# Kernel optimization log

Measured on AMD Instinct MI355X. Metric: run time of the kernel, lower is better.

## Reference

```python
import jax, jax.numpy as jnp
import numpy as np

B, N, C, R = 16, 1024, 256, 8
E = 262144
NUM_SUPER = 32
EPS = 1e-5


def _ln(x, g, b):
    mu = jnp.mean(x, axis=-1, keepdims=True)
    var = jnp.var(x, axis=-1, keepdims=True)
    return (x - mu) / jnp.sqrt(var + EPS) * g + b


def setup_inputs() -> dict:
    key = jax.random.key(0)
    ks = jax.random.split(key, 20)

    def w(k, shape, fan_in):
        return (jax.random.normal(k, shape, jnp.float32) / np.sqrt(fan_in)).astype(jnp.float32)

    return dict(
        x=jax.random.normal(ks[0], (B, N, C), jnp.float32),
        batch_edge_index=jax.random.randint(ks[1], (2, E), 0, B * N),
        batch_edge_types=jax.random.randint(ks[2], (E,), 0, R),
        # cross-modal attention
        Wq=w(ks[3], (C, C), C), bq=jnp.zeros((C,), jnp.float32),
        Wk=w(ks[4], (C, C), C), bk=jnp.zeros((C,), jnp.float32),
        Wv=w(ks[5], (C, C), C), bv=jnp.zeros((C,), jnp.float32),
        Wg=w(ks[6], (2 * C, C), 2 * C), bg=jnp.zeros((C,), jnp.float32),
        ln_attn_g=jnp.ones((C,), jnp.float32), ln_attn_b=jnp.zeros((C,), jnp.float32),
        # confidence net
        Wc1=w(ks[7], (C, C // 2), C), bc1=jnp.zeros((C // 2,), jnp.float32),
        Wc2=w(ks[8], (C // 2, 1), C // 2), bc2=jnp.zeros((1,), jnp.float32),
        # feature mixer
        Wm=w(ks[9], (2 * C, C), 2 * C), bm=jnp.zeros((C,), jnp.float32),
        ln1_g=jnp.ones((C,), jnp.float32), ln1_b=jnp.zeros((C,), jnp.float32),
        # RGCN
        W_rel=w(ks[10], (R, C, C), C),
        W_root=w(ks[11], (C, C), C),
        b_rgcn=jnp.zeros((C,), jnp.float32),
        ln2_g=jnp.ones((C,), jnp.float32), ln2_b=jnp.zeros((C,), jnp.float32),
        # super class head
        Wh=w(ks[12], (C, NUM_SUPER), C), bh=jnp.zeros((NUM_SUPER,), jnp.float32),
    )


def reference(x, batch_edge_index, batch_edge_types,
              Wq, bq, Wk, bk, Wv, bv, Wg, bg, ln_attn_g, ln_attn_b,
              Wc1, bc1, Wc2, bc2, Wm, bm, ln1_g, ln1_b,
              W_rel, W_root, b_rgcn, ln2_g, ln2_b, Wh, bh):
    residual = x
    q = x @ Wq + bq
    k = x @ Wk + bk
    v = x @ Wv + bv
    attn = jax.nn.softmax(jnp.einsum('bnc,bmc->bnm', q, k) / jnp.sqrt(jnp.float32(C)), axis=-1)
    out = jnp.einsum('bnm,bmc->bnc', attn, v)
    gate = jax.nn.sigmoid(jnp.concatenate([out, residual], axis=-1) @ Wg + bg)
    validated = _ln(gate * out + (1.0 - gate) * residual, ln_attn_g, ln_attn_b)

    conf = jax.nn.sigmoid(jax.nn.relu(validated @ Wc1 + bc1) @ Wc2 + bc2)  # [B,N,1]
    weighted = validated * conf
    xm = jax.nn.relu(jnp.concatenate([x, weighted], axis=-1) @ Wm + bm)
    xn = _ln(xm, ln1_g, ln1_b).reshape(B * N, C)

    # RGCNConv (PyG defaults: mean aggregation per relation, root weight, bias)
    src, dst = batch_edge_index[0], batch_edge_index[1]
    h = jnp.einsum('nc,rcd->rnd', xn, W_rel)          # [R, B*N, C] relation-transformed nodes
    msg = h[batch_edge_types, src]                    # [E, C] per-edge gather
    seg = dst * R + batch_edge_types                  # (node, relation) segment id
    cnt = jax.ops.segment_sum(jnp.ones((E,), xn.dtype), seg, num_segments=B * N * R)
    msg = msg / jnp.maximum(cnt[seg], 1.0)[:, None]
    agg = jax.ops.segment_sum(msg, dst, num_segments=B * N)
    x_rgcn = agg + xn @ W_root + b_rgcn
    x_rgcn = jax.nn.relu(_ln(x_rgcn.reshape(B, N, C), ln2_g, ln2_b))

    denom = jnp.maximum(conf.sum(axis=1), 1e-8)       # [B,1]
    pooled = (x_rgcn * conf).sum(axis=1) / denom      # [B,C]
    return pooled @ Wh + bh                           # [B, NUM_SUPER]
```

## Files before the change

kernel.cpp:

```cpp
#include <hip/hip_runtime.h>
#include <hip/hip_bf16.h>

#define B_ 16
#define N_ 1024
#define C_ 256
#define R_ 8
#define E_ 262144
#define NS_ 32
#define BN_ (B_*N_)
#define BNC_ (BN_*C_)

typedef __hip_bfloat16 bf16;
typedef __attribute__((ext_vector_type(4))) float f32x4;
typedef __attribute__((ext_vector_type(8))) short bf16x8;

__device__ __forceinline__ float b2f(bf16 x) { return __bfloat162float(x); }
__device__ __forceinline__ bf16  f2b(float x) { return __float2bfloat16(x); }
__device__ __forceinline__ float us2f(unsigned short u) { return __uint_as_float((unsigned)u << 16); }

__device__ __forceinline__ void gload16(const void* g, void* l) {
    auto gp = (const __attribute__((address_space(1))) void*)(unsigned long long)g;
    auto lp = (__attribute__((address_space(3))) void*)(unsigned)(unsigned long long)l;
    __builtin_amdgcn_global_load_lds(gp, lp, 16, 0, 0);
}

template<int ACT>
__global__ __launch_bounds__(256) void gemm_bf16(
    const bf16* __restrict__ A, int lda, long long sA,
    const bf16* __restrict__ Bm, int ldb, long long sB,
    bf16* __restrict__ Cc, int ldc, long long sC,
    const float* __restrict__ bias, const float* __restrict__ bias2,
    const float* __restrict__ bias3, int K)
{
    __shared__ short sbuf[8704];
    short* As = sbuf;
    short* Bs = sbuf + 4096;
    const int tid = threadIdx.x;
    const int lane = tid & 63, w = tid >> 6;
    const int wr = w >> 1, wc = w & 1;
    const int bm = blockIdx.y * 128, bn = blockIdx.x * 128;
    const bf16* Ab = A + (size_t)blockIdx.z * sA;
    const bf16* Bb = Bm + (size_t)blockIdx.z * sB;
    bf16* Cb = Cc + (size_t)blockIdx.z * sC;

    const int rg = lane >> 2;
    const int kswz = ((lane & 3) ^ ((rg >> 1) & 3)) * 8;

    f32x4 acc[4][4];
    const f32x4 zz = {0.f, 0.f, 0.f, 0.f};
    #pragma unroll
    for (int i = 0; i < 4; ++i)
        #pragma unroll
        for (int j = 0; j < 4; ++j) acc[i][j] = zz;

    const int fr = lane & 15;
    const int fm = lane >> 4;
    const int fslot = (fm ^ ((fr >> 1) & 3)) * 8;

    for (int k0 = 0; k0 < K; k0 += 32) {
        __syncthreads();
        #pragma unroll
        for (int t = 0; t < 2; ++t) {
            gload16(Ab + (size_t)(bm + t*64 + w*16 + rg) * lda + k0 + kswz, As + t*2048 + w*512);
            gload16(Bb + (size_t)(bn + t*64 + w*16 + rg) * ldb + k0 + kswz, Bs + t*2048 + w*512);
        }
        __syncthreads();
        bf16x8 af[4], bfr[4];
        #pragma unroll
        for (int i = 0; i < 4; ++i)
            af[i] = *(const bf16x8*)&As[(wr*64 + i*16 + fr)*32 + fslot];
        #pragma unroll
        for (int j = 0; j < 4; ++j)
            bfr[j] = *(const bf16x8*)&Bs[(wc*64 + j*16 + fr)*32 + fslot];
        #pragma unroll
        for (int i = 0; i < 4; ++i)
            #pragma unroll
            for (int j = 0; j < 4; ++j)
                acc[i][j] = __builtin_amdgcn_mfma_f32_16x16x32_bf16(af[i], bfr[j], acc[i][j], 0, 0, 0);
    }

    const int er = (lane >> 4) * 4, ec = lane & 15;
    #pragma unroll
    for (int half = 0; half < 2; ++half) {
        __syncthreads();
        if (wr == half) {
            #pragma unroll
            for (int j = 0; j < 4; ++j) {
                const int col = bn + wc*64 + j*16 + ec;
                float bvv = 0.0f;
                if (bias) {
                    const int seg = col >> 8;
                    const float* bp = (seg == 0) ? bias : (seg == 1 ? bias2 : bias3);
                    bvv = bp[col & 255];
                }
                #pragma unroll
                for (int i = 0; i < 4; ++i) {
                    #pragma unroll
                    for (int p = 0; p < 4; ++p) {
                        float val = acc[i][j][p] + bvv;
                        if (ACT == 1) val = fmaxf(val, 0.0f);
                        if (ACT == 2) val = 1.0f / (1.0f + __expf(-val));
                        *(bf16*)&sbuf[(i*16 + er + p)*136 + wc*64 + j*16 + ec] = f2b(val);
                    }
                }
            }
        }
        __syncthreads();
        #pragma unroll
        for (int it = 0; it < 4; ++it) {
            const int ch = tid + it*256;
            const int row = ch >> 4, cp = (ch & 15) * 8;
            *(bf16x8*)&Cb[(size_t)(bm + half*64 + row) * ldc + bn + cp] =
                *(const bf16x8*)&sbuf[row*136 + cp];
        }
    }
}

__global__ __launch_bounds__(256) void prep_w_k(
    const float* __restrict__ Wq, const float* __restrict__ Wk, const float* __restrict__ Wv,
    const float* __restrict__ Wg, const float* __restrict__ Wm, const float* __restrict__ Wc1,
    const float* __restrict__ Wrel, const float* __restrict__ Wroot, bf16* __restrict__ WT)
{
    int t = blockIdx.x;
    const float* in; bf16* out; int K, Nn;
    if (t < 192)      { int wsel = t >> 6; t &= 63;
                        in = wsel == 0 ? Wq : (wsel == 1 ? Wk : Wv);
                        out = WT + wsel*65536; K = 256; Nn = 256; }
    else if (t < 320) { t -= 192; in = Wg;  out = WT + 196608; K = 512; Nn = 256; }
    else if (t < 448) { t -= 320; in = Wm;  out = WT + 327680; K = 512; Nn = 256; }
    else if (t < 480) { t -= 448; in = Wc1; out = WT + 458752; K = 256; Nn = 128; }
    else if (t < 992) { t -= 480; int r = t >> 6; t &= 63;
                        in = Wrel + (size_t)r*65536; out = WT + 491520 + r*65536; K = 256; Nn = 256; }
    else              { t -= 992; in = Wroot; out = WT + 491520 + 524288; K = 256; Nn = 256; }
    const int tpr = Nn >> 5;
    const int n0 = (t % tpr) * 32, k0 = (t / tpr) * 32;
    __shared__ float tile[32][33];
    const int tx = threadIdx.x & 31, ty = threadIdx.x >> 5;
    #pragma unroll
    for (int i = 0; i < 4; ++i) {
        int r = ty + i*8;
        tile[r][tx] = in[(size_t)(k0 + r) * Nn + n0 + tx];
    }
    __syncthreads();
    #pragma unroll
    for (int i = 0; i < 4; ++i) {
        int r = ty + i*8;
        out[(size_t)(n0 + r) * K + k0 + tx] = f2b(tile[tx][r]);
    }
}

__global__ __launch_bounds__(256) void vtrans_k(
    const bf16* __restrict__ in, bf16* __restrict__ out)
{
    __shared__ float tile[32][33];
    in  += (size_t)blockIdx.z * 786432 + 512;
    out += (size_t)blockIdx.z * 262144;
    const int n0 = blockIdx.x * 32, k0 = blockIdx.y * 32;
    const int tx = threadIdx.x & 31, ty = threadIdx.x >> 5;
    #pragma unroll
    for (int i = 0; i < 4; ++i) {
        int r = ty + i*8;
        tile[r][tx] = b2f(in[(size_t)(k0 + r) * 768 + n0 + tx]);
    }
    __syncthreads();
    #pragma unroll
    for (int i = 0; i < 4; ++i) {
        int r = ty + i*8;
        out[(size_t)(n0 + r) * 1024 + k0 + tx] = f2b(tile[tx][r]);
    }
}

__global__ __launch_bounds__(256) void cvt_x_k(const float* __restrict__ x,
    bf16* __restrict__ xb, bf16* __restrict__ cat1, bf16* __restrict__ cat2)
{
    const int i4 = (blockIdx.x * 256 + threadIdx.x) * 4;
    const float4 xv = *(const float4*)(x + i4);
    bf16 bv[4] = { f2b(xv.x), f2b(xv.y), f2b(xv.z), f2b(xv.w) };
    const ushort4 pack = *(const ushort4*)bv;
    const int row = i4 >> 8, col = i4 & 255;
    *(ushort4*)(xb + i4) = pack;
    *(ushort4*)(cat1 + (size_t)row * 512 + 256 + col) = pack;
    *(ushort4*)(cat2 + (size_t)row * 512 + col) = pack;
}

__global__ __launch_bounds__(256) void softmax_k(bf16* __restrict__ s)
{
    const int row = blockIdx.x, tid = threadIdx.x;
    const int lane = tid & 63, wid = tid >> 6;
    bf16* rp = s + (size_t)row * 1024 + tid * 4;
    __shared__ float red[8];
    const ushort4 sv = *(const ushort4*)rp;
    float v0 = us2f(sv.x) * 0.0625f, v1 = us2f(sv.y) * 0.0625f;
    float v2 = us2f(sv.z) * 0.0625f, v3 = us2f(sv.w) * 0.0625f;
    float m = fmaxf(fmaxf(v0, v1), fmaxf(v2, v3));
    #pragma unroll
    for (int o = 32; o >= 1; o >>= 1) m = fmaxf(m, __shfl_xor(m, o));
    if (lane == 0) red[wid] = m;
    __syncthreads();
    const float mx = fmaxf(fmaxf(red[0], red[1]), fmaxf(red[2], red[3]));
    float e0 = __expf(v0 - mx), e1 = __expf(v1 - mx), e2 = __expf(v2 - mx), e3 = __expf(v3 - mx);
    float sm = e0 + e1 + e2 + e3;
    #pragma unroll
    for (int o = 32; o >= 1; o >>= 1) sm += __shfl_xor(sm, o);
    if (lane == 0) red[4 + wid] = sm;
    __syncthreads();
    const float inv = 1.0f / (red[4] + red[5] + red[6] + red[7]);
    bf16 ov[4] = { f2b(e0 * inv), f2b(e1 * inv), f2b(e2 * inv), f2b(e3 * inv) };
    *(ushort4*)rp = *(const ushort4*)ov;
}

template<int RELU>
__global__ __launch_bounds__(256) void ln_k(
    const bf16* __restrict__ in, bf16* __restrict__ out,
    const float* __restrict__ g, const float* __restrict__ bta)
{
    const int node = blockIdx.x * 4 + (threadIdx.x >> 6);
    const int lane = threadIdx.x & 63;
    const ushort4 iv = *(const ushort4*)(in + (size_t)node * 256 + lane * 4);
    float v0 = us2f(iv.x), v1 = us2f(iv.y), v2 = us2f(iv.z), v3 = us2f(iv.w);
    float s  = v0 + v1 + v2 + v3;
    float sq = v0*v0 + v1*v1 + v2*v2 + v3*v3;
    #pragma unroll
    for (int o = 32; o >= 1; o >>= 1) { s += __shfl_xor(s, o); sq += __shfl_xor(sq, o); }
    const float mean = s * (1.0f / 256.0f);
    const float var  = sq * (1.0f / 256.0f) - mean * mean;
    const float rs = rsqrtf(var + 1e-5f);
    const float4 gv = *(const float4*)(g + lane * 4);
    const float4 bv = *(const float4*)(bta + lane * 4);
    float y0 = (v0 - mean) * rs * gv.x + bv.x;
    float y1 = (v1 - mean) * rs * gv.y + bv.y;
    float y2 = (v2 - mean) * rs * gv.z + bv.z;
    float y3 = (v3 - mean) * rs * gv.w + bv.w;
    if (RELU) { y0 = fmaxf(y0, 0.f); y1 = fmaxf(y1, 0.f); y2 = fmaxf(y2, 0.f); y3 = fmaxf(y3, 0.f); }
    bf16 ov[4] = { f2b(y0), f2b(y1), f2b(y2), f2b(y3) };
    *(ushort4*)(out + (size_t)node * 256 + lane * 4) = *(const ushort4*)ov;
}

__global__ __launch_bounds__(256) void blend_ln_k(
    const bf16* __restrict__ gate, const bf16* __restrict__ cat1,
    const float* __restrict__ x, bf16* __restrict__ valid,
    const float* __restrict__ g, const float* __restrict__ bta)
{
    const int node = blockIdx.x * 4 + (threadIdx.x >> 6);
    const int lane = threadIdx.x & 63;
    const ushort4 gt4 = *(const ushort4*)(gate + (size_t)node * 256 + lane * 4);
    const ushort4 ao4 = *(const ushort4*)(cat1 + (size_t)node * 512 + lane * 4);
    const float4  xv4 = *(const float4*)(x + (size_t)node * 256 + lane * 4);
    float g0 = us2f(gt4.x), g1 = us2f(gt4.y), g2 = us2f(gt4.z), g3 = us2f(gt4.w);
    float v0 = g0 * us2f(ao4.x) + (1.f - g0) * xv4.x;
    float v1 = g1 * us2f(ao4.y) + (1.f - g1) * xv4.y;
    float v2 = g2 * us2f(ao4.z) + (1.f - g2) * xv4.z;
    float v3 = g3 * us2f(ao4.w) + (1.f - g3) * xv4.w;
    float s  = v0 + v1 + v2 + v3;
    float sq = v0*v0 + v1*v1 + v2*v2 + v3*v3;
    #pragma unroll
    for (int o = 32; o >= 1; o >>= 1) { s += __shfl_xor(s, o); sq += __shfl_xor(sq, o); }
    const float mean = s * (1.0f / 256.0f);
    const float var  = sq * (1.0f / 256.0f) - mean * mean;
    const float rs = rsqrtf(var + 1e-5f);
    const float4 gv = *(const float4*)(g + lane * 4);
    const float4 bv = *(const float4*)(bta + lane * 4);
    bf16 ov[4] = { f2b((v0 - mean) * rs * gv.x + bv.x), f2b((v1 - mean) * rs * gv.y + bv.y),
                   f2b((v2 - mean) * rs * gv.z + bv.z), f2b((v3 - mean) * rs * gv.w + bv.w) };
    *(ushort4*)(valid + (size_t)node * 256 + lane * 4) = *(const ushort4*)ov;
}

__global__ __launch_bounds__(256) void conf_w_k(
    const bf16* __restrict__ t1, const float* __restrict__ Wc2, const float* __restrict__ bc2,
    const bf16* __restrict__ valid, float* __restrict__ conf, bf16* __restrict__ cat2)
{
    const int node = blockIdx.x * 4 + (threadIdx.x >> 6);
    const int lane = threadIdx.x & 63;
    float a = b2f(t1[(size_t)node * 128 + lane]) * Wc2[lane]
            + b2f(t1[(size_t)node * 128 + 64 + lane]) * Wc2[64 + lane];
    #pragma unroll
    for (int o = 32; o >= 1; o >>= 1) a += __shfl_xor(a, o);
    const float c = 1.0f / (1.0f + __expf(-(a + bc2[0])));
    if (lane == 0) conf[node] = c;
    const ushort4 vv = *(const ushort4*)(valid + (size_t)node * 256 + lane * 4);
    bf16 ov[4] = { f2b(us2f(vv.x) * c), f2b(us2f(vv.y) * c), f2b(us2f(vv.z) * c), f2b(us2f(vv.w) * c) };
    *(ushort4*)(cat2 + (size_t)node * 512 + 256 + lane * 4) = *(const ushort4*)ov;
}

__global__ __launch_bounds__(256) void count2_k(
    const int* __restrict__ dst, const int* __restrict__ et,
    int* __restrict__ deg, int* __restrict__ cnt8)
{
    const int e = blockIdx.x * 256 + threadIdx.x;
    if (e < E_) {
        const int d = dst[e];
        atomicAdd(&deg[d], 1);
        atomicAdd(&cnt8[d * 8 + et[e]], 1);
    }
}

__global__ __launch_bounds__(256) void scan_k(
    const int* __restrict__ deg, int* __restrict__ rowptr, int* __restrict__ cursor)
{
    __shared__ int part[256];
    const int tid = threadIdx.x;
    const int base = tid * 64;
    int s = 0;
    for (int i = 0; i < 64; ++i) s += deg[base + i];
    part[tid] = s; __syncthreads();
    for (int off = 1; off < 256; off <<= 1) {
        int t = (tid >= off) ? part[tid - off] : 0;
        __syncthreads();
        part[tid] += t;
        __syncthreads();
    }
    int run = (tid == 0) ? 0 : part[tid - 1];
    for (int i = 0; i < 64; ++i) {
        rowptr[base + i] = run;
        cursor[base + i] = run;
        run += deg[base + i];
    }
    if (tid == 255) rowptr[BN_] = run;
}

__global__ __launch_bounds__(256) void fill_k(
    const int* __restrict__ src, const int* __restrict__ dst, const int* __restrict__ et,
    int* __restrict__ cursor, int* __restrict__ elist)
{
    const int e = blockIdx.x * 256 + threadIdx.x;
    if (e < E_) {
        const int pos = atomicAdd(&cursor[dst[e]], 1);
        elist[pos] = src[e] | (et[e] << 16);
    }
}

__global__ __launch_bounds__(256) void gather_ln_k(
    const int* __restrict__ rowptr, const int* __restrict__ elist,
    const bf16* __restrict__ h, const int* __restrict__ cnt8,
    const float* __restrict__ brg,
    const float* __restrict__ g, const float* __restrict__ bta,
    bf16* __restrict__ xr)
{
    const int node = blockIdx.x * 4 + (threadIdx.x >> 6);
    const int lane = threadIdx.x & 63;
    const int e0 = rowptr[node], e1 = rowptr[node + 1];
    float invc[8];
    #pragma unroll
    for (int r = 0; r < 8; ++r)
        invc[r] = 1.0f / fmaxf((float)cnt8[node * 8 + r], 1.0f);
    float a0 = 0.f, a1 = 0.f, a2 = 0.f, a3 = 0.f;
    for (int e = e0; e < e1; ++e) {
        const int pe = elist[e];
        const int srcn = pe & 0xffff, rel = pe >> 16;
        const float wgt = invc[rel];
        const ushort4 hv = *(const ushort4*)(h + (size_t)srcn * 2304 + rel * 256 + lane * 4);
        a0 += wgt * us2f(hv.x); a1 += wgt * us2f(hv.y);
        a2 += wgt * us2f(hv.z); a3 += wgt * us2f(hv.w);
    }
    const ushort4 rv = *(const ushort4*)(h + (size_t)node * 2304 + 2048 + lane * 4);
    const float4 bg4 = *(const float4*)(brg + lane * 4);
    const float v0 = a0 + us2f(rv.x) + bg4.x, v1 = a1 + us2f(rv.y) + bg4.y;
    const float v2 = a2 + us2f(rv.z) + bg4.z, v3 = a3 + us2f(rv.w) + bg4.w;
    float s  = v0 + v1 + v2 + v3;
    float sq = v0*v0 + v1*v1 + v2*v2 + v3*v3;
    #pragma unroll
    for (int m = 32; m >= 1; m >>= 1) { s += __shfl_xor(s, m); sq += __shfl_xor(sq, m); }
    const float mean = s * (1.0f / 256.0f);
    const float var  = sq * (1.0f / 256.0f) - mean * mean;
    const float rs = rsqrtf(var + 1e-5f);
    const float4 gv = *(const float4*)(g + lane * 4);
    const float4 bv = *(const float4*)(bta + lane * 4);
    bf16 tb[4] = { f2b(fmaxf((v0 - mean) * rs * gv.x + bv.x, 0.f)),
                   f2b(fmaxf((v1 - mean) * rs * gv.y + bv.y, 0.f)),
                   f2b(fmaxf((v2 - mean) * rs * gv.z + bv.z, 0.f)),
                   f2b(fmaxf((v3 - mean) * rs * gv.w + bv.w, 0.f)) };
    *(ushort4*)(xr + (size_t)node * 256 + lane * 4) = *(const ushort4*)tb;
}

__global__ __launch_bounds__(256) void pool1_k(
    const bf16* __restrict__ xr, const float* __restrict__ conf, float* __restrict__ partial)
{
    const int b = blockIdx.x, chunk = blockIdx.y, c = threadIdx.x;
    float acc = 0.0f;
    for (int n = 0; n < 64; ++n) {
        const int node = b * 1024 + chunk * 64 + n;
        acc += conf[node] * b2f(xr[(size_t)node * 256 + c]);
    }
    partial[(size_t)(b * 16 + chunk) * 256 + c] = acc;
}

__global__ __launch_bounds__(256) void pool2_k(
    const float* __restrict__ partial, const float* __restrict__ conf,
    const float* __restrict__ Wh, const float* __restrict__ bh, float* __restrict__ out)
{
    const int b = blockIdx.x, tid = threadIdx.x;
    __shared__ float red[256];
    __shared__ float pooled[256];
    float pc = 0.0f;
    for (int ch = 0; ch < 16; ++ch) pc += partial[(size_t)(b * 16 + ch) * 256 + tid];
    float s = conf[b * 1024 + tid] + conf[b * 1024 + 256 + tid]
            + conf[b * 1024 + 512 + tid] + conf[b * 1024 + 768 + tid];
    red[tid] = s; __syncthreads();
    for (int st = 128; st > 0; st >>= 1) { if (tid < st) red[tid] += red[tid + st]; __syncthreads(); }
    const float denom = fmaxf(red[0], 1e-8f);
    pooled[tid] = pc / denom;
    __syncthreads();
    if (tid < NS_) {
        float o = bh[tid];
        for (int c = 0; c < 256; ++c) o += pooled[c] * Wh[c * NS_ + tid];
        out[b * NS_ + tid] = o;
    }
}

extern "C" void kernel_launch(void* const* d_in, const int* in_sizes, int n_in,
                              void* d_out, int out_size, void* d_ws, size_t ws_size,
                              hipStream_t stream) {
    const float* x    = (const float*)d_in[0];
    const int*   ei   = (const int*)d_in[1];
    const int*   et   = (const int*)d_in[2];
    const float* Wq   = (const float*)d_in[3];  const float* bq  = (const float*)d_in[4];
    const float* Wk   = (const float*)d_in[5];  const float* bk  = (const float*)d_in[6];
    const float* Wv   = (const float*)d_in[7];  const float* bv  = (const float*)d_in[8];
    const float* Wg   = (const float*)d_in[9];  const float* bg  = (const float*)d_in[10];
    const float* lag  = (const float*)d_in[11]; const float* lab = (const float*)d_in[12];
    const float* Wc1  = (const float*)d_in[13]; const float* bc1 = (const float*)d_in[14];
    const float* Wc2  = (const float*)d_in[15]; const float* bc2 = (const float*)d_in[16];
    const float* Wm   = (const float*)d_in[17]; const float* bm  = (const float*)d_in[18];
    const float* l1g  = (const float*)d_in[19]; const float* l1b = (const float*)d_in[20];
    const float* Wrel = (const float*)d_in[21]; const float* Wroot = (const float*)d_in[22];
    const float* brg  = (const float*)d_in[23];
    const float* l2g  = (const float*)d_in[24]; const float* l2b = (const float*)d_in[25];
    const float* Wh   = (const float*)d_in[26]; const float* bh  = (const float*)d_in[27];
    const int* esrc = ei;
    const int* edst = ei + E_;

    char* w8 = (char*)d_ws;
    bf16*  qkv   = (bf16*)(w8 + 0);
    bf16*  hbuf  = (bf16*)(w8 + 0);
    bf16*  sP    = (bf16*)(w8 + 25165824);
    bf16*  cat1  = (bf16*)(w8 + 58720256);
    bf16*  cat2  = (bf16*)(w8 + 75497472);
    bf16*  gate  = (bf16*)(w8 + 92274688);
    bf16*  valid = (bf16*)(w8 + 100663296);
    bf16*  t1    = (bf16*)(w8 + 109051904);
    bf16*  xm    = (bf16*)(w8 + 113246208);
    bf16*  xb    = (bf16*)(w8 + 121634816);
    bf16*  xn    = (bf16*)(w8 + 130023424);
    bf16*  vtb   = (bf16*)(w8 + 138412032);
    bf16*  xr    = (bf16*)(w8 + 146800640);
    float* conf  = (float*)(w8 + 155189248);
    float* part  = (float*)(w8 + 155254784);
    bf16*  WT    = (bf16*)(w8 + 155516928);
    int*  deg    = (int*)(w8 + 157679616);
    int*  cnt8i  = (int*)(w8 + 157745152);
    int*  rowptr = (int*)(w8 + 158269440);
    int*  cursor = (int*)(w8 + 158335232);
    int*  elist  = (int*)(w8 + 158400768);
    bf16* WqkvT = WT;
    bf16* WgT   = WT + 196608;
    bf16* WmT   = WT + 327680;
    bf16* Wc1T  = WT + 458752;
    bf16* WBIG  = WT + 491520;
    float* outp = (float*)d_out;

    dim3 blk(256);

    prep_w_k<<<1056, blk, 0, stream>>>(Wq, Wk, Wv, Wg, Wm, Wc1, Wrel, Wroot, WT);
    cvt_x_k<<<BNC_ / 1024, blk, 0, stream>>>(x, xb, cat1, cat2);
    hipMemsetAsync(deg, 0, 589824, stream);
    count2_k<<<E_ / 256, blk, 0, stream>>>(edst, et, deg, cnt8i);
    scan_k<<<1, blk, 0, stream>>>(deg, rowptr, cursor);
    fill_k<<<E_ / 256, blk, 0, stream>>>(esrc, edst, et, cursor, elist);

    gemm_bf16<0><<<dim3(6, 128, 1), blk, 0, stream>>>(
        xb, 256, 0, WqkvT, 256, 0, qkv, 768, 0, bq, bk, bv, 256);
    vtrans_k<<<dim3(8, 32, 16), blk, 0, stream>>>(qkv, vtb);

    gemm_bf16<0><<<dim3(8, 8, 16), blk, 0, stream>>>(
        qkv, 768, 786432, qkv + 256, 768, 786432, sP, 1024, 1048576, nullptr, nullptr, nullptr, 256);
    softmax_k<<<BN_, blk, 0, stream>>>(sP);
    gemm_bf16<0><<<dim3(2, 8, 16), blk, 0, stream>>>(
        sP, 1024, 1048576, vtb, 1024, 262144, cat1, 512, 524288, nullptr, nullptr, nullptr, 1024);

    gemm_bf16<2><<<dim3(2, 128, 1), blk, 0, stream>>>(
        cat1, 512, 0, WgT, 512, 0, gate, 256, 0, bg, nullptr, nullptr, 512);
    blend_ln_k<<<BN_ / 4, blk, 0, stream>>>(gate, cat1, x, valid, lag, lab);

    gemm_bf16<1><<<dim3(1, 128, 1), blk, 0, stream>>>(
        valid, 256, 0, Wc1T, 256, 0, t1, 128, 0, bc1, nullptr, nullptr, 256);
    conf_w_k<<<BN_ / 4, blk, 0, stream>>>(t1, Wc2, bc2, valid, conf, cat2);

    gemm_bf16<1><<<dim3(2, 128, 1), blk, 0, stream>>>(
        cat2, 512, 0, WmT, 512, 0, xm, 256, 0, bm, nullptr, nullptr, 512);
    ln_k<0><<<BN_ / 4, blk, 0, stream>>>(xm, xn, l1g, l1b);

    gemm_bf16<0><<<dim3(18, 128, 1), blk, 0, stream>>>(
        xn, 256, 0, WBIG, 256, 0, hbuf, 2304, 0, nullptr, nullptr, nullptr, 256);
    gather_ln_k<<<BN_ / 4, blk, 0, stream>>>(rowptr, elist, hbuf, cnt8i, brg, l2g, l2b, xr);

    pool1_k<<<dim3(B_, 16), blk, 0, stream>>>(xr, conf, part);
    pool2_k<<<B_, blk, 0, stream>>>(part, conf, Wh, bh, outp);
}
```

Baseline: 315.8 us.

## Double-buffer GEMM LDS tiles with async global-to-LDS prefetch two stages ahead

Turns the bf16 MFMA GEMM main loop into a two-stage double-buffered pipeline. Global-to-LDS loads for the k-tile two steps ahead are issued as soon as the current fragments are in registers, and explicit vmcnt/lgkmcnt waits replace the full syncthreads pairs. This is meant to hide global load latency behind MFMA work, at the cost of doubling LDS per block, which may lower occupancy.

```diff
diff --git a/kernel.cpp b/kernel.cpp
--- a/kernel.cpp
+++ b/kernel.cpp
@@ -32,9 +32,7 @@
     const float* __restrict__ bias, const float* __restrict__ bias2,
     const float* __restrict__ bias3, int K)
 {
-    __shared__ short sbuf[8704];
-    short* As = sbuf;
-    short* Bs = sbuf + 4096;
+    __shared__ short sbuf[16384];
     const int tid = threadIdx.x;
     const int lane = tid & 63, w = tid >> 6;
     const int wr = w >> 1, wc = w & 1;
@@ -57,32 +55,54 @@
     const int fm = lane >> 4;
     const int fslot = (fm ^ ((fr >> 1) & 3)) * 8;
 
-    for (int k0 = 0; k0 < K; k0 += 32) {
-        __syncthreads();
+    const int NI = K >> 5;
+
+#define STAGE_AB(bi, kk) do {                                                          \
+    _Pragma("unroll")                                                                  \
+    for (int t_ = 0; t_ < 2; ++t_) {                                                   \
+        gload16(Ab + (size_t)(bm + t_*64 + w*16 + rg) * lda + (kk) + kswz,             \
+                sbuf + (bi)*4096 + t_*2048 + w*512);                                   \
+        gload16(Bb + (size_t)(bn + t_*64 + w*16 + rg) * ldb + (kk) + kswz,             \
+                sbuf + 8192 + (bi)*4096 + t_*2048 + w*512);                            \
+    } } while (0)
+
+    STAGE_AB(0, 0);
+    if (NI > 1) STAGE_AB(1, 32);
+
+    for (int i = 0; i < NI; ++i) {
+        const int cur = i & 1;
+        if (i + 1 < NI) asm volatile("s_waitcnt vmcnt(4)" ::: "memory");
+        else            asm volatile("s_waitcnt vmcnt(0)" ::: "memory");
+        __builtin_amdgcn_s_barrier();
+        __builtin_amdgcn_sched_barrier(0);
+
+        bf16x8 af[4], bfr[4];
+        const short* Ac = sbuf + cur * 4096;
+        const short* Bc = sbuf + 8192 + cur * 4096;
         #pragma unroll
-        for (int t = 0; t < 2; ++t) {
-            gload16(Ab + (size_t)(bm + t*64 + w*16 + rg) * lda + k0 + kswz, As + t*2048 + w*512);
-            gload16(Bb + (size_t)(bn + t*64 + w*16 + rg) * ldb + k0 + kswz, Bs + t*2048 + w*512);
-        }
-        __syncthreads();
-        bf16x8 af[4], bfr[4];
+        for (int ii = 0; ii < 4; ++ii)
+            af[ii] = *(const bf16x8*)&Ac[(wr*64 + ii*16 + fr)*32 + fslot];
         #pragma unroll
-        for (int i = 0; i < 4; ++i)
-            af[i] = *(const bf16x8*)&As[(wr*64 + i*16 + fr)*32 + fslot];
+        for (int jj = 0; jj < 4; ++jj)
+            bfr[jj] = *(const bf16x8*)&Bc[(wc*64 + jj*16 + fr)*32 + fslot];
+
+        asm volatile("s_waitcnt lgkmcnt(0)" ::: "memory");
+        __builtin_amdgcn_s_barrier();
+        __builtin_amdgcn_sched_barrier(0);
+        if (i + 2 < NI) STAGE_AB(cur, (i + 2) * 32);
+
         #pragma unroll
-        for (int j = 0; j < 4; ++j)
-            bfr[j] = *(const bf16x8*)&Bs[(wc*64 + j*16 + fr)*32 + fslot];
-        #pragma unroll
-        for (int i = 0; i < 4; ++i)
+        for (int ii = 0; ii < 4; ++ii)
             #pragma unroll
-            for (int j = 0; j < 4; ++j)
-                acc[i][j] = __builtin_amdgcn_mfma_f32_16x16x32_bf16(af[i], bfr[j], acc[i][j], 0, 0, 0);
-    }
-
+            for (int jj = 0; jj < 4; ++jj)
+                acc[ii][jj] = __builtin_amdgcn_mfma_f32_16x16x32_bf16(af[ii], bfr[jj], acc[ii][jj], 0, 0, 0);
+    }
+#undef STAGE_AB
+
+    __syncthreads();
     const int er = (lane >> 4) * 4, ec = lane & 15;
     #pragma unroll
     for (int half = 0; half < 2; ++half) {
-        __syncthreads();
         if (wr == half) {
             #pragma unroll
             for (int j = 0; j < 4; ++j) {
@@ -113,6 +133,7 @@
             *(bf16x8*)&Cb[(size_t)(bm + half*64 + row) * ldc + bn + cp] =
                 *(const bf16x8*)&sbuf[row*136 + cp];
         }
+        __syncthreads();
     }
 }
 
```

After: 283.9 us. -10.1%, faster.
